# Kernel tuning notes

Hardware: AMD Instinct MI355X
Metric: run time of the kernel (lower is better)

## Reference

```python
import jax, jax.numpy as jnp
import numpy as np

B = 262144
MA = [128, 128]
MB = [128, 128]


def krone_linear(x_a, x_b, wa, wb, ba, bb):
    # slice inputs to each branch's in_features (torch slices the wider branch)
    ia, ib = wa.shape[1], wb.shape[1]
    x_a = x_a[:, :ia]
    x_b = x_b[:, :ib]
    h_a = x_a @ wa.T + ba
    h_b = x_b @ wb.T + bb
    # zero-pad the narrower output so both branches share a width (static shapes)
    oa, ob = wa.shape[0], wb.shape[0]
    if oa > ob:
        h_b = jnp.pad(h_b, ((0, 0), (0, oa - ob)))
    elif ob > oa:
        h_a = jnp.pad(h_a, ((0, 0), (0, ob - oa)))
    return h_a, h_b


def krone_softmax(x_a, x_b, fa, fb):
    x_a = x_a[:, :fa]
    x_b = x_b[:, :fb]
    # vectorized per-row Kronecker product: kron(a, b)[i*fb + j] = a[i]*b[j]
    y = (x_a[:, :, None] * x_b[:, None, :]).reshape(x_a.shape[0], fa * fb)
    return jax.nn.softmax(y, axis=1)


def setup_inputs() -> dict:
    key = jax.random.key(0)
    ks = jax.random.split(key, 13)
    s = 0.1
    inp = {
        "x": jax.random.normal(ks[0], (2, B, 2), dtype=jnp.float32),
        "w1a": jax.random.normal(ks[1], (MA[0], 2), dtype=jnp.float32) * s,
        "w1b": jax.random.normal(ks[2], (MB[0], 2), dtype=jnp.float32) * s,
        "b1a": jax.random.normal(ks[3], (MA[0],), dtype=jnp.float32) * s,
        "b1b": jax.random.normal(ks[4], (MB[0],), dtype=jnp.float32) * s,
        "w2a": jax.random.normal(ks[5], (MA[1], MA[0]), dtype=jnp.float32) * s,
        "w2b": jax.random.normal(ks[6], (MB[1], MB[0]), dtype=jnp.float32) * s,
        "b2a": jax.random.normal(ks[7], (MA[1],), dtype=jnp.float32) * s,
        "b2b": jax.random.normal(ks[8], (MB[1],), dtype=jnp.float32) * s,
        "w3a": jax.random.normal(ks[9], (1, MA[1]), dtype=jnp.float32) * s,
        "w3b": jax.random.normal(ks[10], (3, MB[1]), dtype=jnp.float32) * s,
        "b3a": jax.random.normal(ks[11], (1,), dtype=jnp.float32) * s,
        "b3b": jax.random.normal(ks[12], (3,), dtype=jnp.float32) * s,
    }
    return inp


def reference(x, w1a, w1b, b1a, b1b, w2a, w2b, b2a, b2b, w3a, w3b, b3a, b3b):
    x_a, x_b = x[0], x[1]
    h_a, h_b = krone_linear(x_a, x_b, w1a, w1b, b1a, b1b)
    h_a, h_b = jax.nn.relu(h_a), jax.nn.relu(h_b)
    h_a, h_b = krone_linear(h_a, h_b, w2a, w2b, b2a, b2b)
    h_a, h_b = jax.nn.relu(h_a), jax.nn.relu(h_b)
    h_a, h_b = krone_linear(h_a, h_b, w3a, w3b, b3a, b3b)
    return krone_softmax(h_a, h_b, 1, 3)
```

## Files before the change

### kernel.cpp

```cpp
#include <hip/hip_runtime.h>
#include <hip/hip_bf16.h>


#define BTOT 262144
#define NBLK (BTOT / 256)

typedef __attribute__((ext_vector_type(4))) float floatx4;
typedef __attribute__((ext_vector_type(8))) short bf16x8;
typedef __attribute__((ext_vector_type(4))) int  intx4;

#define OFF_W2  0
#define OFF_W1  65536
#define OFF_B2  70144
#define OFF_W3A 71168
#define OFF_W3B 71680
#define OFF_B3  73216
#define WS_TOTAL 73232

static __device__ __forceinline__ short f2bf(float f) {
    __hip_bfloat16 h = __float2bfloat16(f);
    return __builtin_bit_cast(short, h);
}

static __device__ __forceinline__ int pack2bf(float lo, float hi) {
    unsigned a = __builtin_bit_cast(unsigned, lo) + 0x8000u;
    unsigned b = __builtin_bit_cast(unsigned, hi) + 0x8000u;
    return (int)__builtin_amdgcn_perm(b, a, 0x07060302u);
}

#define SEL4(a0, a1, a2, a3, i) \
    ((i) == 0 ? (a0) : (i) == 1 ? (a1) : (i) == 2 ? (a2) : (a3))

static __device__ __forceinline__ float redcol(float v) {
    v += __shfl_xor(v, 1); v += __shfl_xor(v, 2);
    v += __shfl_xor(v, 4); v += __shfl_xor(v, 8);
    return v;
}

static __device__ __forceinline__ int w1slot(int k) { return k + (k >> 3); }

__global__ void pack_kernel(const float* __restrict__ w1a, const float* __restrict__ w1b,
                            const float* __restrict__ b1a, const float* __restrict__ b1b,
                            const float* __restrict__ w2a, const float* __restrict__ w2b,
                            const float* __restrict__ b2a, const float* __restrict__ b2b,
                            const float* __restrict__ w3a, const float* __restrict__ w3b,
                            const float* __restrict__ b3a, const float* __restrict__ b3b,
                            unsigned char* __restrict__ ws) {
    const int b = blockIdx.x;
    const int tid = threadIdx.x;
    const int path = b >> 5;
    const int r = b & 31;
    const int s = r >> 3;
    const int t = r & 7;
    const float* w2 = path ? w2b : w2a;
    unsigned short* pk = (unsigned short*)(ws + OFF_W2 + path * 32768 + ((s * 8 + t) * 64) * 16);
    #pragma unroll
    for (int q = 0; q < 2; ++q) {
        int e = tid * 2 + q;
        int l = e >> 3, j = e & 7;
        int n = t * 16 + (l & 15);
        int k = s * 32 + ((l >> 4) * 8) + j;
        pk[e] = (unsigned short)f2bf(w2[n * 128 + k]);
    }
    if (b == 0) {
        {
            int pth = tid >> 7, k = tid & 127;
            const float* w1 = pth ? w1b : w1a;
            const float* b1 = pth ? b1b : b1a;
            ((float4*)(ws + OFF_W1))[pth * 144 + w1slot(k)] =
                make_float4(w1[2 * k], w1[2 * k + 1], b1[k], 0.f);
            ((float*)(ws + OFF_B2))[tid] = (pth ? b2b : b2a)[k];
        }
        if (tid < 128) ((float*)(ws + OFF_W3A))[tid] = w3a[tid];
        for (int i = tid; i < 384; i += 256) ((float*)(ws + OFF_W3B))[i] = w3b[i];
        if (tid == 0) {
            float* d = (float*)(ws + OFF_B3);
            d[0] = b3a[0]; d[1] = b3b[0]; d[2] = b3b[1]; d[3] = b3b[2];
        }
    }
}

__global__ __launch_bounds__(256, 2)
void krone_main(const float* __restrict__ x, const unsigned char* __restrict__ ws,
                float* __restrict__ out) {
    __shared__ __align__(16) unsigned char smem[WS_TOTAL];
    __shared__ float4 sEx[4][32];

    const int tid = threadIdx.x;
    {
        const float4* src = (const float4*)ws;
        float4* dst = (float4*)smem;
        for (int i = tid; i < WS_TOTAL / 16; i += 256) dst[i] = src[i];
    }
    __syncthreads();

    const int lane = tid & 63;
    const int wave = tid >> 6;
    const int quad = lane >> 4;
    const int col  = lane & 15;

    const bf16x8* W2A = (const bf16x8*)(smem + OFF_W2);
    const bf16x8* W2B = (const bf16x8*)(smem + OFF_W2 + 32768);
    const float4* W1A = (const float4*)(smem + OFF_W1);
    const float4* W1B = W1A + 144;
    const float*  B2A = (const float*)(smem + OFF_B2);
    const float*  B2B = B2A + 128;
    const float*  W3A = (const float*)(smem + OFF_W3A);
    const float*  W3B = (const float*)(smem + OFF_W3B);
    const float*  B3  = (const float*)(smem + OFF_B3);
    const float2* xA  = (const float2*)x;
    const float2* xB  = xA + BTOT;

    #pragma unroll
    for (int c = 0; c < 2; ++c) {
        __builtin_amdgcn_sched_barrier(0);
        const int base = blockIdx.x * 256 + wave * 64 + c * 32;

        float2 xa[2], xb[2];
        #pragma unroll
        for (int mt = 0; mt < 2; ++mt) {
            xa[mt] = xA[base + mt * 16 + col];
            xb[mt] = xB[base + mt * 16 + col];
        }

        floatx4 accA[8][2], accB[8][2];
        #pragma unroll
        for (int t = 0; t < 8; ++t)
            #pragma unroll
            for (int mt = 0; mt < 2; ++mt) {
                accA[t][mt] = (floatx4){0.f, 0.f, 0.f, 0.f};
                accB[t][mt] = (floatx4){0.f, 0.f, 0.f, 0.f};
            }

        #pragma unroll
        for (int s = 0; s < 4; ++s) {
            intx4 afA[2], afB[2];
            const int bslot = s * 36 + quad * 9;
            #pragma unroll
            for (int j2 = 0; j2 < 4; ++j2) {
                float4 a0 = W1A[bslot + 2 * j2];
                float4 a1 = W1A[bslot + 2 * j2 + 1];
                float4 b0 = W1B[bslot + 2 * j2];
                float4 b1 = W1B[bslot + 2 * j2 + 1];
                #pragma unroll
                for (int mt = 0; mt < 2; ++mt) {
                    float ha0 = fmaxf(fmaf(xa[mt].x, a0.x, fmaf(xa[mt].y, a0.y, a0.z)), 0.f);
                    float ha1 = fmaxf(fmaf(xa[mt].x, a1.x, fmaf(xa[mt].y, a1.y, a1.z)), 0.f);
                    float hb0 = fmaxf(fmaf(xb[mt].x, b0.x, fmaf(xb[mt].y, b0.y, b0.z)), 0.f);
                    float hb1 = fmaxf(fmaf(xb[mt].x, b1.x, fmaf(xb[mt].y, b1.y, b1.z)), 0.f);
                    afA[mt][j2] = pack2bf(ha0, ha1);
                    afB[mt][j2] = pack2bf(hb0, hb1);
                }
            }
            #pragma unroll
            for (int t = 0; t < 8; ++t) {
                bf16x8 bfa = W2A[(s * 8 + t) * 64 + lane];
                bf16x8 bfb = W2B[(s * 8 + t) * 64 + lane];
                #pragma unroll
                for (int mt = 0; mt < 2; ++mt) {
                    accA[t][mt] = __builtin_amdgcn_mfma_f32_16x16x32_bf16(
                        __builtin_bit_cast(bf16x8, afA[mt]), bfa, accA[t][mt], 0, 0, 0);
                    accB[t][mt] = __builtin_amdgcn_mfma_f32_16x16x32_bf16(
                        __builtin_bit_cast(bf16x8, afB[mt]), bfb, accB[t][mt], 0, 0, 0);
                }
            }
        }
        __builtin_amdgcn_sched_barrier(0);

        float pa[2][4]  = {};
        float pb0[2][4] = {}, pb1[2][4] = {}, pb2[2][4] = {};
        #pragma unroll
        for (int t = 0; t < 8; ++t) {
            int n = t * 16 + col;
            float b2a = B2A[n], w3a = W3A[n];
            float b2b = B2B[n];
            float w30 = W3B[n], w31 = W3B[128 + n], w32 = W3B[256 + n];
            #pragma unroll
            for (int mt = 0; mt < 2; ++mt)
                #pragma unroll
                for (int r = 0; r < 4; ++r) {
                    float ha = fmaxf(accA[t][mt][r] + b2a, 0.f);
                    pa[mt][r] = fmaf(w3a, ha, pa[mt][r]);
                    float hb = fmaxf(accB[t][mt][r] + b2b, 0.f);
                    pb0[mt][r] = fmaf(w30, hb, pb0[mt][r]);
                    pb1[mt][r] = fmaf(w31, hb, pb1[mt][r]);
                    pb2[mt][r] = fmaf(w32, hb, pb2[mt][r]);
                }
        }
        #pragma unroll
        for (int mt = 0; mt < 2; ++mt)
            #pragma unroll
            for (int r = 0; r < 4; ++r) {
                pa[mt][r]  = redcol(pa[mt][r]);
                pb0[mt][r] = redcol(pb0[mt][r]);
                pb1[mt][r] = redcol(pb1[mt][r]);
                pb2[mt][r] = redcol(pb2[mt][r]);
            }
        __builtin_amdgcn_sched_barrier(0);

        if (col < 4) {
            float b3a = B3[0], b30 = B3[1], b31 = B3[2], b32 = B3[3];
            #pragma unroll
            for (int mt = 0; mt < 2; ++mt) {
                int sl = mt * 16 + quad * 4 + col;
                float va = SEL4(pa[mt][0],  pa[mt][1],  pa[mt][2],  pa[mt][3],  col) + b3a;
                float v0 = SEL4(pb0[mt][0], pb0[mt][1], pb0[mt][2], pb0[mt][3], col) + b30;
                float v1 = SEL4(pb1[mt][0], pb1[mt][1], pb1[mt][2], pb1[mt][3], col) + b31;
                float v2 = SEL4(pb2[mt][0], pb2[mt][1], pb2[mt][2], pb2[mt][3], col) + b32;
                sEx[wave][sl] = make_float4(va, v0, v1, v2);
            }
        }
        if (lane < 32) {
            float4 v = sEx[wave][lane];
            float y0 = v.x * v.y, y1 = v.x * v.z, y2 = v.x * v.w;
            float m = fmaxf(y0, fmaxf(y1, y2));
            float e0 = __expf(y0 - m), e1 = __expf(y1 - m), e2 = __expf(y2 - m);
            float rs = 1.f / (e0 + e1 + e2);
            long o = (long)(base + lane) * 3;
            out[o]     = e0 * rs;
            out[o + 1] = e1 * rs;
            out[o + 2] = e2 * rs;
        }
        __builtin_amdgcn_sched_barrier(0);
    }
}

extern "C" void kernel_launch(void* const* d_in, const int* in_sizes, int n_in,
                              void* d_out, int out_size, void* d_ws, size_t ws_size,
                              hipStream_t stream) {
    const float* x   = (const float*)d_in[0];
    const float* w1a = (const float*)d_in[1];
    const float* w1b = (const float*)d_in[2];
    const float* b1a = (const float*)d_in[3];
    const float* b1b = (const float*)d_in[4];
    const float* w2a = (const float*)d_in[5];
    const float* w2b = (const float*)d_in[6];
    const float* b2a = (const float*)d_in[7];
    const float* b2b = (const float*)d_in[8];
    const float* w3a = (const float*)d_in[9];
    const float* w3b = (const float*)d_in[10];
    const float* b3a = (const float*)d_in[11];
    const float* b3b = (const float*)d_in[12];
    unsigned char* ws = (unsigned char*)d_ws;
    float* out = (float*)d_out;

    pack_kernel<<<64, 256, 0, stream>>>(w1a, w1b, b1a, b1b, w2a, w2b,
                                        b2a, b2b, w3a, w3b, b3a, b3b, ws);
    krone_main<<<NBLK, 256, 0, stream>>>(x, ws, out);
}
```

Measured before the change: 120.1 us.

## Fuse weight packing into main kernel and use 512-thread blocks

Removes the separate pack kernel. Each block of the main kernel now reads the fp32 weights directly, converts W2 to bf16 in the MFMA fragment layout and writes the result into shared memory. Blocks grow to 512 threads (8 waves) and cover 512 rows, so half as many blocks are launched and the per-block weight staging is spread over more rows. In exchange, every block repeats the fp32-to-bf16 conversion and reads twice the weight bytes (fp32 instead of packed bf16), and the launch bounds change to (512, 4).

```diff
diff --git a/kernel.cpp b/kernel.cpp
--- a/kernel.cpp
+++ b/kernel.cpp
@@ -3,7 +3,7 @@
 
 
 #define BTOT 262144
-#define NBLK (BTOT / 256)
+#define NBLK (BTOT / 512)
 
 typedef __attribute__((ext_vector_type(4))) float floatx4;
 typedef __attribute__((ext_vector_type(8))) short bf16x8;
@@ -17,11 +17,6 @@
 #define OFF_B3  73216
 #define WS_TOTAL 73232
 
-static __device__ __forceinline__ short f2bf(float f) {
-    __hip_bfloat16 h = __float2bfloat16(f);
-    return __builtin_bit_cast(short, h);
-}
-
 static __device__ __forceinline__ int pack2bf(float lo, float hi) {
     unsigned a = __builtin_bit_cast(unsigned, lo) + 0x8000u;
     unsigned b = __builtin_bit_cast(unsigned, hi) + 0x8000u;
@@ -39,58 +34,58 @@
 
 static __device__ __forceinline__ int w1slot(int k) { return k + (k >> 3); }
 
-__global__ void pack_kernel(const float* __restrict__ w1a, const float* __restrict__ w1b,
-                            const float* __restrict__ b1a, const float* __restrict__ b1b,
-                            const float* __restrict__ w2a, const float* __restrict__ w2b,
-                            const float* __restrict__ b2a, const float* __restrict__ b2b,
-                            const float* __restrict__ w3a, const float* __restrict__ w3b,
-                            const float* __restrict__ b3a, const float* __restrict__ b3b,
-                            unsigned char* __restrict__ ws) {
-    const int b = blockIdx.x;
+__global__ __launch_bounds__(512, 4)
+void krone_main(const float* __restrict__ x,
+                const float* __restrict__ w1a, const float* __restrict__ w1b,
+                const float* __restrict__ b1a, const float* __restrict__ b1b,
+                const float* __restrict__ w2a, const float* __restrict__ w2b,
+                const float* __restrict__ b2a, const float* __restrict__ b2b,
+                const float* __restrict__ w3a, const float* __restrict__ w3b,
+                const float* __restrict__ b3a, const float* __restrict__ b3b,
+                float* __restrict__ out) {
+    __shared__ __align__(16) unsigned char smem[WS_TOTAL];
+    __shared__ float4 sEx[8][32];
+
     const int tid = threadIdx.x;
-    const int path = b >> 5;
-    const int r = b & 31;
-    const int s = r >> 3;
-    const int t = r & 7;
-    const float* w2 = path ? w2b : w2a;
-    unsigned short* pk = (unsigned short*)(ws + OFF_W2 + path * 32768 + ((s * 8 + t) * 64) * 16);
-    #pragma unroll
-    for (int q = 0; q < 2; ++q) {
-        int e = tid * 2 + q;
-        int l = e >> 3, j = e & 7;
-        int n = t * 16 + (l & 15);
-        int k = s * 32 + ((l >> 4) * 8) + j;
-        pk[e] = (unsigned short)f2bf(w2[n * 128 + k]);
-    }
-    if (b == 0) {
-        {
-            int pth = tid >> 7, k = tid & 127;
+
+    {
+        #pragma unroll
+        for (int i = 0; i < 16; ++i) {
+            int u = i * 512 + tid;
+            int path = u >> 12;
+            int v = u & 4095;
+            int n = v >> 5;
+            int k4 = v & 31;
+            const float4* w2p = (const float4*)(path ? w2b : w2a);
+            float4 f = w2p[n * 32 + k4];
+            int k = k4 * 4;
+            int s = k >> 5;
+            int quad = (k & 31) >> 3;
+            int j0 = k & 7;
+            int tt = n >> 4;
+            int l = quad * 16 + (n & 15);
+            int2 pkd;
+            pkd.x = pack2bf(f.x, f.y);
+            pkd.y = pack2bf(f.z, f.w);
+            *(int2*)(smem + OFF_W2 + path * 32768 + (s * 8 + tt) * 1024 + l * 16 + j0 * 2) = pkd;
+        }
+        if (tid < 256) {
+            int pth = tid >> 7, kk = tid & 127;
             const float* w1 = pth ? w1b : w1a;
             const float* b1 = pth ? b1b : b1a;
-            ((float4*)(ws + OFF_W1))[pth * 144 + w1slot(k)] =
-                make_float4(w1[2 * k], w1[2 * k + 1], b1[k], 0.f);
-            ((float*)(ws + OFF_B2))[tid] = (pth ? b2b : b2a)[k];
-        }
-        if (tid < 128) ((float*)(ws + OFF_W3A))[tid] = w3a[tid];
-        for (int i = tid; i < 384; i += 256) ((float*)(ws + OFF_W3B))[i] = w3b[i];
+            ((float4*)(smem + OFF_W1))[pth * 144 + w1slot(kk)] =
+                make_float4(w1[2 * kk], w1[2 * kk + 1], b1[kk], 0.f);
+            ((float*)(smem + OFF_B2))[tid] = (pth ? b2b : b2a)[kk];
+        } else if (tid < 384) {
+            ((float*)(smem + OFF_W3A))[tid - 256] = w3a[tid - 256];
+        }
+        if (tid >= 128) {
+            ((float*)(smem + OFF_W3B))[tid - 128] = w3b[tid - 128];
+        }
         if (tid == 0) {
-            float* d = (float*)(ws + OFF_B3);
+            float* d = (float*)(smem + OFF_B3);
             d[0] = b3a[0]; d[1] = b3b[0]; d[2] = b3b[1]; d[3] = b3b[2];
         }
-    }
-}
-
-__global__ __launch_bounds__(256, 2)
-void krone_main(const float* __restrict__ x, const unsigned char* __restrict__ ws,
-                float* __restrict__ out) {
-    __shared__ __align__(16) unsigned char smem[WS_TOTAL];
-    __shared__ float4 sEx[4][32];
-
-    const int tid = threadIdx.x;
-    {
-        const float4* src = (const float4*)ws;
-        float4* dst = (float4*)smem;
-        for (int i = tid; i < WS_TOTAL / 16; i += 256) dst[i] = src[i];
     }
     __syncthreads();
 
@@ -114,7 +109,7 @@
     #pragma unroll
     for (int c = 0; c < 2; ++c) {
         __builtin_amdgcn_sched_barrier(0);
-        const int base = blockIdx.x * 256 + wave * 64 + c * 32;
+        const int base = blockIdx.x * 512 + c * 256 + wave * 32;
 
         float2 xa[2], xb[2];
         #pragma unroll
@@ -172,16 +167,16 @@
         #pragma unroll
         for (int t = 0; t < 8; ++t) {
             int n = t * 16 + col;
-            float b2a = B2A[n], w3a = W3A[n];
-            float b2b = B2B[n];
+            float b2a_ = B2A[n], w3a_ = W3A[n];
+            float b2b_ = B2B[n];
             float w30 = W3B[n], w31 = W3B[128 + n], w32 = W3B[256 + n];
             #pragma unroll
             for (int mt = 0; mt < 2; ++mt)
                 #pragma unroll
                 for (int r = 0; r < 4; ++r) {
-                    float ha = fmaxf(accA[t][mt][r] + b2a, 0.f);
-                    pa[mt][r] = fmaf(w3a, ha, pa[mt][r]);
-                    float hb = fmaxf(accB[t][mt][r] + b2b, 0.f);
+                    float ha = fmaxf(accA[t][mt][r] + b2a_, 0.f);
+                    pa[mt][r] = fmaf(w3a_, ha, pa[mt][r]);
+                    float hb = fmaxf(accB[t][mt][r] + b2b_, 0.f);
                     pb0[mt][r] = fmaf(w30, hb, pb0[mt][r]);
                     pb1[mt][r] = fmaf(w31, hb, pb1[mt][r]);
                     pb2[mt][r] = fmaf(w32, hb, pb2[mt][r]);
@@ -199,11 +194,11 @@
         __builtin_amdgcn_sched_barrier(0);
 
         if (col < 4) {
-            float b3a = B3[0], b30 = B3[1], b31 = B3[2], b32 = B3[3];
+            float b3a_ = B3[0], b30 = B3[1], b31 = B3[2], b32 = B3[3];
             #pragma unroll
             for (int mt = 0; mt < 2; ++mt) {
                 int sl = mt * 16 + quad * 4 + col;
-                float va = SEL4(pa[mt][0],  pa[mt][1],  pa[mt][2],  pa[mt][3],  col) + b3a;
+                float va = SEL4(pa[mt][0],  pa[mt][1],  pa[mt][2],  pa[mt][3],  col) + b3a_;
                 float v0 = SEL4(pb0[mt][0], pb0[mt][1], pb0[mt][2], pb0[mt][3], col) + b30;
                 float v1 = SEL4(pb1[mt][0], pb1[mt][1], pb1[mt][2], pb1[mt][3], col) + b31;
                 float v2 = SEL4(pb2[mt][0], pb2[mt][1], pb2[mt][2], pb2[mt][3], col) + b32;
@@ -241,10 +236,8 @@
     const float* w3b = (const float*)d_in[10];
     const float* b3a = (const float*)d_in[11];
     const float* b3b = (const float*)d_in[12];
-    unsigned char* ws = (unsigned char*)d_ws;
     float* out = (float*)d_out;
 
-    pack_kernel<<<64, 256, 0, stream>>>(w1a, w1b, b1a, b1b, w2a, w2b,
-                                        b2a, b2b, w3a, w3b, b3a, b3b, ws);
-    krone_main<<<NBLK, 256, 0, stream>>>(x, ws, out);
-}
+    krone_main<<<NBLK, 512, 0, stream>>>(x, w1a, w1b, b1a, b1b, w2a, w2b,
+                                         b2a, b2b, w3a, w3b, b3a, b3b, out);
+}
```

New measurement: 222.5 us. 85.2% more time.
